# Kernel optimization log

Hardware: AMD Instinct MI355X
Metric: run time of the kernel (lower is better)

## Reference

```python
import jax, jax.numpy as jnp
import numpy as np

NC = 80          # class_num
THRESH = 0.5     # objectness threshold (forward arg `thresh`)
IOU_T = 0.3      # NMS IoU threshold (utils.nms(boxes_c, 0.3))
K = 512          # fixed candidate budget per image (jit-safe replacement for nonzero)


def _decode(out, t, anchors):
    """_filter + _parse for one scale. out: (B, 3*(5+NC), H, W) -> boxes (B, H*W*3, 6), conf (B, H*W*3).
    Box columns: x1, y1, x2, y2, conf, cls."""
    B, C, H, W = out.shape
    o = out.transpose(0, 2, 3, 1).reshape(B, H, W, 3, 5 + NC)
    txy = jax.nn.sigmoid(o[..., 0:2])          # sigmoid on tx, ty
    conf = jax.nn.sigmoid(o[..., 4])           # sigmoid on objectness
    gy = jnp.arange(H, dtype=out.dtype)[:, None, None]   # grid row index (idxs[:,1])
    gx = jnp.arange(W, dtype=out.dtype)[None, :, None]   # grid col index (idxs[:,2])
    cy = (gy + txy[..., 1]) * t
    cx = (gx + txy[..., 0]) * t
    w = anchors[:, 0] * jnp.exp(o[..., 2])     # anchors broadcast over anchor axis
    h = anchors[:, 1] * jnp.exp(o[..., 3])
    cls = jnp.argmax(o[..., 5:], axis=-1).astype(out.dtype)
    boxes = jnp.stack([cx - w / 2, cy - h / 2, cx + w / 2, cy + h / 2, conf, cls], axis=-1)
    return boxes.reshape(B, -1, 6), conf.reshape(B, -1)


def _iou(b):
    """Pairwise IoU. b: (B, K, 4) -> (B, K, K)."""
    x1, y1, x2, y2 = b[..., 0], b[..., 1], b[..., 2], b[..., 3]
    area = (x2 - x1) * (y2 - y1)
    ix1 = jnp.maximum(x1[:, :, None], x1[:, None, :])
    iy1 = jnp.maximum(y1[:, :, None], y1[:, None, :])
    ix2 = jnp.minimum(x2[:, :, None], x2[:, None, :])
    iy2 = jnp.minimum(y2[:, :, None], y2[:, None, :])
    inter = jnp.maximum(ix2 - ix1, 0.0) * jnp.maximum(iy2 - iy1, 0.0)
    return inter / (area[:, :, None] + area[:, None, :] - inter + 1e-9)


def setup_inputs() -> dict:
    key = jax.random.key(0)
    k1, k2, k3 = jax.random.split(key, 3)
    B, C = 32, 3 * (5 + NC)
    return {
        "out13": jax.random.normal(k1, (B, C, 13, 13), jnp.float32),
        "out26": jax.random.normal(k2, (B, C, 26, 26), jnp.float32),
        "out52": jax.random.normal(k3, (B, C, 52, 52), jnp.float32),
        "anchors13": jnp.array([[116.0, 90.0], [156.0, 198.0], [373.0, 326.0]], jnp.float32),
        "anchors26": jnp.array([[30.0, 61.0], [62.0, 45.0], [59.0, 119.0]], jnp.float32),
        "anchors52": jnp.array([[10.0, 13.0], [16.0, 30.0], [33.0, 23.0]], jnp.float32),
    }


def reference(out13, out26, out52, anchors13, anchors26, anchors52):
    b13, c13 = _decode(out13, 32.0, anchors13)
    b26, c26 = _decode(out26, 16.0, anchors26)
    b52, c52 = _decode(out52, 8.0, anchors52)
    boxes = jnp.concatenate([b13, b26, b52], axis=1)   # (B, N, 6), N = 3549*3
    conf = jnp.concatenate([c13, c26, c52], axis=1)    # (B, N)
    B = boxes.shape[0]

    # threshold filter (conf > thresh) realized as masked top-K (jit-safe nonzero)
    scores = jnp.where(conf > THRESH, conf, -1.0)
    vals, idx = jax.lax.top_k(scores, K)               # sorted descending, as utils.nms expects
    bk = jnp.take_along_axis(boxes, idx[..., None], axis=1)   # (B, K, 6)
    valid = vals > THRESH                              # (B, K)

    # per-class greedy NMS
    iou = _iou(bk[..., :4])                            # (B, K, K)
    same_cls = bk[..., 5][:, :, None] == bk[..., 5][:, None, :]
    suppress = same_cls & (iou > IOU_T)

    def step(keep, i):
        sup_i = jnp.any(keep & suppress[:, i, :], axis=-1)
        keep = keep.at[:, i].set(valid[:, i] & ~sup_i)
        return keep, None

    keep, _ = jax.lax.scan(step, jnp.zeros((B, K), dtype=bool), jnp.arange(K))
    # (B, K, 7): x1, y1, x2, y2, conf, cls, keep_flag
    return jnp.concatenate([bk, keep[..., None].astype(bk.dtype)], axis=-1)
```

## Files before the change

kernel.cpp:

```cpp
#include <hip/hip_runtime.h>
#include <stdint.h>

#define NC13 507
#define NC26 2028
#define NC52 8112
#define NCAND 10647
#define KSEL 512
#define POOLCAP 4096
#define SUPW 17
#define CMW 17
#define DECB 6

__device__ __forceinline__ unsigned long long cand_key(
    int i, int b,
    const float* __restrict__ in13,
    const float* __restrict__ in26,
    const float* __restrict__ in52)
{
    const float* in; int HW, base;
    if (i < NC13)              { in = in13; HW = 169;  base = 0; }
    else if (i < NC13 + NC26)  { in = in26; HW = 676;  base = NC13; }
    else                       { in = in52; HW = 2704; base = NC13 + NC26; }
    const int within = i - base;
    const int a  = within / HW;
    const int hw = within - a * HW;
    const float xo = in[((size_t)b * 255 + (size_t)a * 85 + 4) * HW + hw];
    const int n = base + hw * 3 + a;
    const unsigned long long low = (unsigned long long)(0x3FFFu - (unsigned)n);
    return (xo > 0.0f)
        ? ((1ull << 63) | ((unsigned long long)__float_as_uint(xo) << 32) | low)
        : low;
}

struct SelShared {
    unsigned int hist[4096];
    unsigned long long pool[POOLCAP];
    unsigned int cnt;
    unsigned long long prefix;
    unsigned long long tmin;
    int krem, shift, brk, V;
};

__device__ __forceinline__ void decode_write(
    float* __restrict__ o, int w, int h, float ts,
    float tx, float ty, float tw, float th, float xo,
    float aw, float ah, int cls)
{
    const float sx   = 1.0f / (1.0f + expf(-tx));
    const float sy   = 1.0f / (1.0f + expf(-ty));
    const float conf = 1.0f / (1.0f + expf(-xo));
    const float cx = ((float)w + sx) * ts;
    const float cy = ((float)h + sy) * ts;
    const float bw = aw * expf(tw);
    const float bh = ah * expf(th);
    o[0] = cx - bw * 0.5f; o[1] = cy - bh * 0.5f;
    o[2] = cx + bw * 0.5f; o[3] = cy + bh * 0.5f;
    o[4] = conf; o[5] = (float)cls;
}

__global__ __launch_bounds__(1024) void main_kernel(
    const float* __restrict__ in13,
    const float* __restrict__ in26,
    const float* __restrict__ in52,
    const float* __restrict__ a13,
    const float* __restrict__ a26,
    const float* __restrict__ a52,
    int B,
    int* __restrict__ selidx,
    int* __restrict__ selv,
    float* __restrict__ boxesAll)
{
    __shared__ __align__(16) char smem_raw[sizeof(SelShared)];
    const int bid = blockIdx.x;
    const int tid = threadIdx.x;

    if (bid < B) {
        SelShared& S = *reinterpret_cast<SelShared*>(smem_raw);
        const int b = bid;
        if (tid == 0) { S.cnt = 0; S.prefix = 0; S.krem = KSEL; S.shift = 52; S.brk = 0; S.V = 0; }
        __syncthreads();

        for (int i = tid; i < NCAND; i += 1024) {
            const unsigned long long k = cand_key(i, b, in13, in26, in52);
            const unsigned long long bal = __ballot((k >> 63) != 0ull);
            if ((tid & 63) == 0) atomicAdd(&S.V, (int)__popcll(bal));
        }
        __syncthreads();
        const bool include = (S.V < KSEL);

        while (true) {
            const int shift = S.shift;
            const unsigned long long prefix = S.prefix;
            const int krem = S.krem;
            __syncthreads();
            for (int i = tid; i < 4096; i += 1024) S.hist[i] = 0;
            __syncthreads();
            for (int i = tid; i < NCAND; i += 1024) {
                const unsigned long long k = cand_key(i, b, in13, in26, in52);
                const bool part = include || ((k >> 63) != 0ull);
                const bool ok = part &&
                    ((shift == 52) || ((k >> (shift + 12)) == prefix));
                if (ok) atomicAdd(&S.hist[(unsigned)((k >> shift) & 0xFFFull)], 1u);
            }
            __syncthreads();
            if (tid < 64) {
                unsigned int s = 0;
                for (int q = 0; q < 64; ++q) s += S.hist[tid * 64 + q];
                unsigned int suf = s;
                for (int off = 1; off < 64; off <<= 1) {
                    const unsigned int v = __shfl_down(suf, off);
                    if (tid + off < 64) suf += v;
                }
                const unsigned long long ball = __ballot(suf >= (unsigned)krem);
                const int lstar = 63 - __clzll(ball);
                const unsigned int base = (lstar < 63) ? __shfl(suf, lstar + 1) : 0u;
                const unsigned int wv = S.hist[lstar * 64 + (63 - tid)];
                unsigned int pv = wv;
                for (int off = 1; off < 64; off <<= 1) {
                    const unsigned int v = __shfl_up(pv, off);
                    if (tid >= (unsigned)off) pv += v;
                }
                const unsigned long long b2 = __ballot(base + pv >= (unsigned)krem);
                const int mstar = __ffsll(b2) - 1;
                const unsigned int pvm = __shfl(pv, mstar);
                const unsigned int wvm = __shfl(wv, mstar);
                if (tid == 0) {
                    const int dstar = lstar * 64 + (63 - mstar);
                    const unsigned long long np = (prefix << 12) | (unsigned long long)dstar;
                    const int Albl = (int)(base + pvm - wvm);
                    const int Cpool = (KSEL - krem) + Albl + (int)wvm;
                    S.prefix = np;
                    S.krem = krem - Albl;
                    if (Cpool <= POOLCAP || shift == 4) {
                        S.brk = 1;
                        S.tmin = np << shift;
                    } else {
                        S.shift = shift - 12;
                    }
                }
            }
            __syncthreads();
            if (S.brk) break;
        }
        const unsigned long long tmin = S.tmin;

        for (int i = tid; i < NCAND; i += 1024) {
            const unsigned long long k = cand_key(i, b, in13, in26, in52);
            if (k >= tmin) {
                const unsigned int p = atomicAdd(&S.cnt, 1u);
                if (p < POOLCAP) S.pool[p] = k;
            }
        }
        __syncthreads();
        const int C = ((int)S.cnt < POOLCAP) ? (int)S.cnt : POOLCAP;

        for (int p = tid; p < C; p += 1024) {
            const unsigned long long k = S.pool[p];
            int r = 0;
            for (int j = 0; j < C; ++j) r += (S.pool[j] > k) ? 1 : 0;
            if (r < KSEL) {
                const int idx = 0x3FFF - (int)(k & 0x3FFFull);
                selidx[(size_t)b * KSEL + r] = idx;
                selv[(size_t)b * KSEL + r]   = (int)(k >> 63);
            }
        }
        return;
    }

    const int d = bid - B;
    const int b = d / DECB;
    const int role = d - b * DECB;

    if (role == 0) {
        if (tid >= NC13) return;
        const int HW = 169;
        const int a = tid / HW, hw = tid - a * HW;
        const int h = hw / 13, w = hw - h * 13;
        const float* p = in13 + ((size_t)b * 255 + (size_t)a * 85) * HW + hw;
        float best = p[(size_t)5 * HW]; int bi = 0;
        #pragma unroll 16
        for (int c = 1; c < 80; ++c) {
            const float v = p[(size_t)(5 + c) * HW];
            if (v > best) { best = v; bi = c; }
        }
        const int i = a * HW + hw;
        decode_write(boxesAll + ((size_t)b * NCAND + i) * 6, w, h, 32.f,
                     p[0], p[(size_t)HW], p[(size_t)2 * HW], p[(size_t)3 * HW],
                     p[(size_t)4 * HW], a13[2 * a], a13[2 * a + 1], bi);
        return;
    }

    const float* in; const float* anch; int HW, base, idx2; float ts; int Hdim;
    if (role == 1) {
        if (tid >= NC26 / 2) return;
        in = in26; anch = a26; HW = 676;  base = NC13; ts = 16.f; Hdim = 26; idx2 = tid;
    } else {
        idx2 = (role - 2) * 1024 + tid;
        if (idx2 >= NC52 / 2) return;
        in = in52; anch = a52; HW = 2704; base = NC13 + NC26; ts = 8.f; Hdim = 52;
    }
    const int HW2 = HW / 2;
    const int a = idx2 / HW2;
    const int hw = (idx2 - a * HW2) * 2;
    const float2* p2 = reinterpret_cast<const float2*>(
        in + ((size_t)b * 255 + (size_t)a * 85) * HW + hw);

    const float2 txv = p2[0];
    const float2 tyv = p2[(size_t)HW2];
    const float2 twv = p2[(size_t)2 * HW2];
    const float2 thv = p2[(size_t)3 * HW2];
    const float2 xov = p2[(size_t)4 * HW2];

    float2 best = p2[(size_t)5 * HW2];
    int bix = 0, biy = 0;
    #pragma unroll 16
    for (int c = 1; c < 80; ++c) {
        const float2 v = p2[(size_t)(5 + c) * HW2];
        if (v.x > best.x) { best.x = v.x; bix = c; }
        if (v.y > best.y) { best.y = v.y; biy = c; }
    }

    const int h0 = hw / Hdim, w0 = hw - h0 * Hdim;
    const int hw1 = hw + 1;
    const int h1 = hw1 / Hdim, w1 = hw1 - h1 * Hdim;
    const float aw = anch[2 * a], ah = anch[2 * a + 1];
    const int i0 = base + a * HW + hw;
    float* o = boxesAll + ((size_t)b * NCAND + i0) * 6;
    decode_write(o,     w0, h0, ts, txv.x, tyv.x, twv.x, thv.x, xov.x, aw, ah, bix);
    decode_write(o + 6, w1, h1, ts, txv.y, tyv.y, twv.y, thv.y, xov.y, aw, ah, biy);
}

__global__ __launch_bounds__(512) void nms_kernel(
    const float* __restrict__ boxesAll,
    const int* __restrict__ selidx,
    const int* __restrict__ selv,
    float* __restrict__ out)
{
    __shared__ float X1[KSEL], Y1[KSEL], X2[KSEL], Y2[KSEL], AR[KSEL];
    __shared__ int CLS[KSEL];
    __shared__ unsigned int CM[80 * CMW];
    __shared__ unsigned int SUP[KSEL * SUPW];
    __shared__ unsigned int KEEP[16];
    __shared__ int shV;

    const int b = blockIdx.x;
    const int tid = threadIdx.x;

    const int n = selidx[(size_t)b * KSEL + tid];
    int base, HW;
    if (n < NC13)             { base = 0;           HW = 169; }
    else if (n < NC13 + NC26) { base = NC13;        HW = 676; }
    else                      { base = NC13 + NC26; HW = 2704; }
    const int within = n - base;
    const int hw = within / 3, a = within - 3 * hw;
    const int i = base + a * HW + hw;
    const float* src = boxesAll + ((size_t)b * NCAND + i) * 6;
    const float x1 = src[0], y1 = src[1], x2 = src[2], y2 = src[3];
    const float conf = src[4], clsf = src[5];
    const float ar = (x2 - x1) * (y2 - y1);
    const int ci = (int)clsf;
    X1[tid] = x1; Y1[tid] = y1; X2[tid] = x2; Y2[tid] = y2;
    AR[tid] = ar; CLS[tid] = ci;
    const int v = selv[(size_t)b * KSEL + tid];
    if (tid == 0) shV = 0;
    for (int q = tid; q < 80 * CMW; q += KSEL) CM[q] = 0;
    __syncthreads();

    atomicOr(&CM[ci * CMW + (tid >> 5)], 1u << (tid & 31));
    const unsigned long long bal = __ballot(v != 0);
    if ((tid & 63) == 0) atomicAdd(&shV, __popcll(bal));
    __syncthreads();

    for (int wj = 0; wj < 16; ++wj) {
        unsigned int m = CM[ci * CMW + wj];
        unsigned int bits = 0;
        while (m) {
            const int bit = __ffs(m) - 1;
            m &= m - 1;
            const int j = wj * 32 + bit;
            const float iw = fminf(x2, X2[j]) - fmaxf(x1, X1[j]);
            const float ih = fminf(y2, Y2[j]) - fmaxf(y1, Y1[j]);
            if (iw > 0.0f && ih > 0.0f) {
                const float inter = iw * ih;
                if (inter > 0.3f * (ar + AR[j] - inter + 1e-9f))
                    bits |= (1u << bit);
            }
        }
        SUP[tid * SUPW + wj] = bits;
    }
    __syncthreads();

    if (tid < 64) {
        const int V = shV;
        unsigned int keepw = 0;
        unsigned int buf[16];
        #pragma unroll
        for (int r = 0; r < 16; ++r)
            buf[r] = (tid < 16) ? SUP[r * SUPW + tid] : 0u;
        for (int g = 0; g < 32; ++g) {
            unsigned int nbuf[16] = {0};
            if (g < 31) {
                #pragma unroll
                for (int r = 0; r < 16; ++r)
                    nbuf[r] = (tid < 16) ? SUP[((g + 1) * 16 + r) * SUPW + tid] : 0u;
            }
            #pragma unroll
            for (int r = 0; r < 16; ++r) {
                const int ii = g * 16 + r;
                const bool anysup = __any((keepw & buf[r]) != 0u);
                const bool ki = (ii < V) && !anysup;
                if (ki && tid == (ii >> 5)) keepw |= (1u << (ii & 31));
            }
            #pragma unroll
            for (int r = 0; r < 16; ++r) buf[r] = nbuf[r];
        }
        if (tid < 16) KEEP[tid] = keepw;
    }
    __syncthreads();

    const float kf = ((KEEP[tid >> 5] >> (tid & 31)) & 1u) ? 1.0f : 0.0f;
    float* dst = out + ((size_t)b * KSEL + tid) * 7;
    dst[0] = x1; dst[1] = y1; dst[2] = x2;
    dst[3] = y2; dst[4] = conf; dst[5] = clsf;
    dst[6] = kf;
}

extern "C" void kernel_launch(void* const* d_in, const int* in_sizes, int n_in,
                              void* d_out, int out_size, void* d_ws, size_t ws_size,
                              hipStream_t stream)
{
    (void)n_in; (void)out_size; (void)ws_size;
    const float* in13 = (const float*)d_in[0];
    const float* in26 = (const float*)d_in[1];
    const float* in52 = (const float*)d_in[2];
    const float* a13  = (const float*)d_in[3];
    const float* a26  = (const float*)d_in[4];
    const float* a52  = (const float*)d_in[5];
    float* out = (float*)d_out;
    const int B = in_sizes[0] / (255 * 169);

    char* w = (char*)d_ws;
    int* selidx = (int*)w;  w += ((size_t)B * KSEL * sizeof(int) + 255) & ~(size_t)255;
    int* selv   = (int*)w;  w += ((size_t)B * KSEL * sizeof(int) + 255) & ~(size_t)255;
    float* boxesAll = (float*)w;
    w += ((size_t)B * NCAND * 6 * sizeof(float) + 255) & ~(size_t)255;

    main_kernel<<<dim3(B * (1 + DECB)), 1024, 0, stream>>>(
        in13, in26, in52, a13, a26, a52, B, selidx, selv, boxesAll);
    nms_kernel<<<dim3(B), 512, 0, stream>>>(boxesAll, selidx, selv, out);
}
```

Measured before the change: 69.23 us.

## Shrink blocks to 256 threads and vectorize decode with float4 and prefetched class loads

The fused select/decode kernel now launches 256-thread blocks. Decode work is spread over 12 blocks per image. Each decode thread handles four cells via float4 loads, with software-prefetched class scores in batches of eight. The selection pool cap is halved to shrink shared memory and the O(C²) rank work. The risk is that the per-image selection block now has a quarter of the threads for its histogram and rank loops, which may lengthen the critical path.

```diff
diff --git a/kernel.cpp b/kernel.cpp
--- a/kernel.cpp
+++ b/kernel.cpp
@@ -6,10 +6,10 @@
 #define NC52 8112
 #define NCAND 10647
 #define KSEL 512
-#define POOLCAP 4096
+#define POOLCAP 2048
 #define SUPW 17
 #define CMW 17
-#define DECB 6
+#define DECB 12
 
 __device__ __forceinline__ unsigned long long cand_key(
     int i, int b,
@@ -58,7 +58,67 @@
     o[4] = conf; o[5] = (float)cls;
 }
 
-__global__ __launch_bounds__(1024) void main_kernel(
+__device__ __forceinline__ void decode4(
+    const float* __restrict__ in, const float* __restrict__ anch,
+    int b, int a, int hw, int HW, int Hdim, float ts, int base,
+    float* __restrict__ boxesAll)
+{
+    const int HW4 = HW >> 2;
+    const float4* p4 = reinterpret_cast<const float4*>(
+        in + ((size_t)b * 255 + (size_t)a * 85) * HW + hw);
+
+    const float4 txv = p4[0];
+    const float4 tyv = p4[(size_t)HW4];
+    const float4 twv = p4[(size_t)2 * HW4];
+    const float4 thv = p4[(size_t)3 * HW4];
+    const float4 xov = p4[(size_t)4 * HW4];
+
+    float4 best = make_float4(-INFINITY, -INFINITY, -INFINITY, -INFINITY);
+    int bx = 0, by = 0, bz = 0, bw4 = 0;
+
+    float4 vb[8];
+    #pragma unroll
+    for (int j = 0; j < 8; ++j) vb[j] = p4[(size_t)(5 + j) * HW4];
+    for (int cb = 0; cb < 10; ++cb) {
+        float4 vn[8];
+        if (cb < 9) {
+            #pragma unroll
+            for (int j = 0; j < 8; ++j) vn[j] = p4[(size_t)(13 + cb * 8 + j) * HW4];
+        }
+        #pragma unroll
+        for (int j = 0; j < 8; ++j) {
+            const int c = cb * 8 + j;
+            if (vb[j].x > best.x) { best.x = vb[j].x; bx = c; }
+            if (vb[j].y > best.y) { best.y = vb[j].y; by = c; }
+            if (vb[j].z > best.z) { best.z = vb[j].z; bz = c; }
+            if (vb[j].w > best.w) { best.w = vb[j].w; bw4 = c; }
+        }
+        #pragma unroll
+        for (int j = 0; j < 8; ++j) vb[j] = vn[j];
+    }
+
+    const float aw = anch[2 * a], ah = anch[2 * a + 1];
+    const int i0 = base + a * HW + hw;
+    float* o = boxesAll + ((size_t)b * NCAND + i0) * 6;
+    {
+        const int h = hw / Hdim, w = hw - h * Hdim;
+        decode_write(o, w, h, ts, txv.x, tyv.x, twv.x, thv.x, xov.x, aw, ah, bx);
+    }
+    {
+        const int h = (hw + 1) / Hdim, w = (hw + 1) - h * Hdim;
+        decode_write(o + 6, w, h, ts, txv.y, tyv.y, twv.y, thv.y, xov.y, aw, ah, by);
+    }
+    {
+        const int h = (hw + 2) / Hdim, w = (hw + 2) - h * Hdim;
+        decode_write(o + 12, w, h, ts, txv.z, tyv.z, twv.z, thv.z, xov.z, aw, ah, bz);
+    }
+    {
+        const int h = (hw + 3) / Hdim, w = (hw + 3) - h * Hdim;
+        decode_write(o + 18, w, h, ts, txv.w, tyv.w, twv.w, thv.w, xov.w, aw, ah, bw4);
+    }
+}
+
+__global__ void main_kernel(
     const float* __restrict__ in13,
     const float* __restrict__ in26,
     const float* __restrict__ in52,
@@ -80,7 +140,7 @@
         if (tid == 0) { S.cnt = 0; S.prefix = 0; S.krem = KSEL; S.shift = 52; S.brk = 0; S.V = 0; }
         __syncthreads();
 
-        for (int i = tid; i < NCAND; i += 1024) {
+        for (int i = tid; i < NCAND; i += 256) {
             const unsigned long long k = cand_key(i, b, in13, in26, in52);
             const unsigned long long bal = __ballot((k >> 63) != 0ull);
             if ((tid & 63) == 0) atomicAdd(&S.V, (int)__popcll(bal));
@@ -93,9 +153,9 @@
             const unsigned long long prefix = S.prefix;
             const int krem = S.krem;
             __syncthreads();
-            for (int i = tid; i < 4096; i += 1024) S.hist[i] = 0;
+            for (int i = tid; i < 4096; i += 256) S.hist[i] = 0;
             __syncthreads();
-            for (int i = tid; i < NCAND; i += 1024) {
+            for (int i = tid; i < NCAND; i += 256) {
                 const unsigned long long k = cand_key(i, b, in13, in26, in52);
                 const bool part = include || ((k >> 63) != 0ull);
                 const bool ok = part &&
@@ -144,7 +204,7 @@
         }
         const unsigned long long tmin = S.tmin;
 
-        for (int i = tid; i < NCAND; i += 1024) {
+        for (int i = tid; i < NCAND; i += 256) {
             const unsigned long long k = cand_key(i, b, in13, in26, in52);
             if (k >= tmin) {
                 const unsigned int p = atomicAdd(&S.cnt, 1u);
@@ -154,7 +214,7 @@
         __syncthreads();
         const int C = ((int)S.cnt < POOLCAP) ? (int)S.cnt : POOLCAP;
 
-        for (int p = tid; p < C; p += 1024) {
+        for (int p = tid; p < C; p += 256) {
             const unsigned long long k = S.pool[p];
             int r = 0;
             for (int j = 0; j < C; ++j) r += (S.pool[j] > k) ? 1 : 0;
@@ -171,63 +231,53 @@
     const int b = d / DECB;
     const int role = d - b * DECB;
 
-    if (role == 0) {
-        if (tid >= NC13) return;
-        const int HW = 169;
-        const int a = tid / HW, hw = tid - a * HW;
-        const int h = hw / 13, w = hw - h * 13;
-        const float* p = in13 + ((size_t)b * 255 + (size_t)a * 85) * HW + hw;
-        float best = p[(size_t)5 * HW]; int bi = 0;
-        #pragma unroll 16
-        for (int c = 1; c < 80; ++c) {
-            const float v = p[(size_t)(5 + c) * HW];
-            if (v > best) { best = v; bi = c; }
-        }
-        const int i = a * HW + hw;
-        decode_write(boxesAll + ((size_t)b * NCAND + i) * 6, w, h, 32.f,
-                     p[0], p[(size_t)HW], p[(size_t)2 * HW], p[(size_t)3 * HW],
-                     p[(size_t)4 * HW], a13[2 * a], a13[2 * a + 1], bi);
-        return;
-    }
-
-    const float* in; const float* anch; int HW, base, idx2; float ts; int Hdim;
-    if (role == 1) {
-        if (tid >= NC26 / 2) return;
-        in = in26; anch = a26; HW = 676;  base = NC13; ts = 16.f; Hdim = 26; idx2 = tid;
+    if (role < 8) {
+        const int idx4 = role * 256 + tid;
+        if (idx4 < 3 * 676) {
+            const int a = idx4 / 676, g = idx4 - a * 676;
+            decode4(in52, a52, b, a, g * 4, 2704, 52, 8.f, NC13 + NC26, boxesAll);
+        }
+    } else if (role < 10) {
+        const int idx4 = (role - 8) * 256 + tid;
+        if (idx4 < 3 * 169) {
+            const int a = idx4 / 169, g = idx4 - a * 169;
+            decode4(in26, a26, b, a, g * 4, 676, 26, 16.f, NC13, boxesAll);
+        }
     } else {
-        idx2 = (role - 2) * 1024 + tid;
-        if (idx2 >= NC52 / 2) return;
-        in = in52; anch = a52; HW = 2704; base = NC13 + NC26; ts = 8.f; Hdim = 52;
-    }
-    const int HW2 = HW / 2;
-    const int a = idx2 / HW2;
-    const int hw = (idx2 - a * HW2) * 2;
-    const float2* p2 = reinterpret_cast<const float2*>(
-        in + ((size_t)b * 255 + (size_t)a * 85) * HW + hw);
-
-    const float2 txv = p2[0];
-    const float2 tyv = p2[(size_t)HW2];
-    const float2 twv = p2[(size_t)2 * HW2];
-    const float2 thv = p2[(size_t)3 * HW2];
-    const float2 xov = p2[(size_t)4 * HW2];
-
-    float2 best = p2[(size_t)5 * HW2];
-    int bix = 0, biy = 0;
-    #pragma unroll 16
-    for (int c = 1; c < 80; ++c) {
-        const float2 v = p2[(size_t)(5 + c) * HW2];
-        if (v.x > best.x) { best.x = v.x; bix = c; }
-        if (v.y > best.y) { best.y = v.y; biy = c; }
-    }
-
-    const int h0 = hw / Hdim, w0 = hw - h0 * Hdim;
-    const int hw1 = hw + 1;
-    const int h1 = hw1 / Hdim, w1 = hw1 - h1 * Hdim;
-    const float aw = anch[2 * a], ah = anch[2 * a + 1];
-    const int i0 = base + a * HW + hw;
-    float* o = boxesAll + ((size_t)b * NCAND + i0) * 6;
-    decode_write(o,     w0, h0, ts, txv.x, tyv.x, twv.x, thv.x, xov.x, aw, ah, bix);
-    decode_write(o + 6, w1, h1, ts, txv.y, tyv.y, twv.y, thv.y, xov.y, aw, ah, biy);
+        const int idx = (role - 10) * 256 + tid;
+        if (idx < NC13) {
+            const int HW = 169;
+            const int a = idx / HW, hw = idx - a * HW;
+            const int h = hw / 13, w = hw - h * 13;
+            const float* p = in13 + ((size_t)b * 255 + (size_t)a * 85) * HW + hw;
+            const float tx = p[0];
+            const float ty = p[(size_t)HW];
+            const float tw = p[(size_t)2 * HW];
+            const float th = p[(size_t)3 * HW];
+            const float xo = p[(size_t)4 * HW];
+            float best = -INFINITY; int bi = 0;
+            float vb[8];
+            #pragma unroll
+            for (int j = 0; j < 8; ++j) vb[j] = p[(size_t)(5 + j) * HW];
+            for (int cb = 0; cb < 10; ++cb) {
+                float vn[8];
+                if (cb < 9) {
+                    #pragma unroll
+                    for (int j = 0; j < 8; ++j) vn[j] = p[(size_t)(13 + cb * 8 + j) * HW];
+                }
+                #pragma unroll
+                for (int j = 0; j < 8; ++j) {
+                    const int c = cb * 8 + j;
+                    if (vb[j] > best) { best = vb[j]; bi = c; }
+                }
+                #pragma unroll
+                for (int j = 0; j < 8; ++j) vb[j] = vn[j];
+            }
+            const int i = a * HW + hw;
+            decode_write(boxesAll + ((size_t)b * NCAND + i) * 6, w, h, 32.f,
+                         tx, ty, tw, th, xo, a13[2 * a], a13[2 * a + 1], bi);
+        }
+    }
 }
 
 __global__ __launch_bounds__(512) void nms_kernel(
@@ -345,7 +395,7 @@
     float* boxesAll = (float*)w;
     w += ((size_t)B * NCAND * 6 * sizeof(float) + 255) & ~(size_t)255;
 
-    main_kernel<<<dim3(B * (1 + DECB)), 1024, 0, stream>>>(
+    main_kernel<<<dim3(B * (1 + DECB)), 256, 0, stream>>>(
         in13, in26, in52, a13, a26, a52, B, selidx, selv, boxesAll);
     nms_kernel<<<dim3(B), 512, 0, stream>>>(boxesAll, selidx, selv, out);
 }
```

Measured after the change: 116.3 us. 1.68x slower.
